# Optimization experiments

Measured on AMD Instinct MI355X. Metric: run time of the kernel, lower is better.

## Reference

```python
import jax, jax.numpy as jnp
import numpy as np

B, T = 32, 64
STOCH, DETER, HIDDEN = 1024, 4096, 1024
ACT_DIM, EMBED = 128, 1536
MIN_STD = 0.1
EPS = 1e-3  # dreamerv3-torch uses LayerNorm(eps=1e-3)


def _ln(x, g, b):
    m = jnp.mean(x, -1, keepdims=True)
    v = jnp.var(x, -1, keepdims=True)
    return (x - m) * jax.lax.rsqrt(v + EPS) * g + b


def setup_inputs() -> dict:
    key = jax.random.key(0)
    ks = jax.random.split(key, 24)

    def w(k, fan_in, fan_out):
        return jax.random.normal(k, (fan_in, fan_out), jnp.float32) / np.sqrt(fan_in)

    inp = {
        "embed": jax.random.normal(ks[0], (B, T, EMBED), jnp.float32),
        "action": jax.random.normal(ks[1], (B, T, ACT_DIM), jnp.float32),
        "is_first": jnp.zeros((B, T), jnp.bool_),
        "init_deter": jax.random.normal(ks[2], (B, DETER), jnp.float32),
        "init_stoch": jax.random.normal(ks[3], (B, STOCH), jnp.float32),
        "noise_prior": jax.random.normal(ks[4], (B, T, STOCH), jnp.float32),
        "noise_post": jax.random.normal(ks[5], (B, T, STOCH), jnp.float32),
        # _img_in_layers: Linear(stoch+act -> hidden, no bias) + LN + SiLU
        "W_in": w(ks[6], STOCH + ACT_DIM, HIDDEN),
        "g_in": 1.0 + 0.1 * jax.random.normal(ks[7], (HIDDEN,), jnp.float32),
        "b_in": 0.1 * jax.random.normal(ks[8], (HIDDEN,), jnp.float32),
        # GRUCell: Linear(hidden+deter -> 3*deter, no bias) + LN
        "W_gru": w(ks[9], HIDDEN + DETER, 3 * DETER),
        "g_gru": 1.0 + 0.1 * jax.random.normal(ks[10], (3 * DETER,), jnp.float32),
        "b_gru": 0.1 * jax.random.normal(ks[11], (3 * DETER,), jnp.float32),
        # _img_out_layers: Linear(deter -> hidden, no bias) + LN + SiLU
        "W_imgout": w(ks[12], DETER, HIDDEN),
        "g_io": 1.0 + 0.1 * jax.random.normal(ks[13], (HIDDEN,), jnp.float32),
        "b_io": 0.1 * jax.random.normal(ks[14], (HIDDEN,), jnp.float32),
        # _obs_out_layers: Linear(deter+embed -> hidden, no bias) + LN + SiLU
        "W_obsout": w(ks[15], DETER + EMBED, HIDDEN),
        "g_oo": 1.0 + 0.1 * jax.random.normal(ks[16], (HIDDEN,), jnp.float32),
        "b_oo": 0.1 * jax.random.normal(ks[17], (HIDDEN,), jnp.float32),
        # suff-stats layers: Linear(hidden -> 2*stoch) with bias
        "W_ims": w(ks[18], HIDDEN, 2 * STOCH),
        "b_ims": 0.01 * jax.random.normal(ks[19], (2 * STOCH,), jnp.float32),
        "W_obs": w(ks[20], HIDDEN, 2 * STOCH),
        "b_obs": 0.01 * jax.random.normal(ks[21], (2 * STOCH,), jnp.float32),
    }
    return inp


def _observe(embed, action, init_deter, init_stoch, noise_prior, noise_post,
             W_in, g_in, b_in, W_gru, g_gru, b_gru, W_imgout, g_io, b_io,
             W_obsout, g_oo, b_oo, W_ims, b_ims, W_obs, b_obs):
    def suff_stats(h, W, b, noise):
        stats = h @ W + b
        mean, std = jnp.split(stats, 2, -1)
        std = jax.nn.softplus(std) + MIN_STD  # std_act='softplus', mean_act='none'
        return mean, std, mean + std * noise

    def step(carry, xs):
        deter, stoch = carry
        e, a, n_p, n_q = xs
        # img_in: concat(prev_stoch, action) -> Linear -> LN -> SiLU
        x = jax.nn.silu(_ln(jnp.concatenate([stoch, a], -1) @ W_in, g_in, b_in))
        # GRUCell with layernorm (update_bias = -1)
        parts = _ln(jnp.concatenate([x, deter], -1) @ W_gru, g_gru, b_gru)
        reset, cand, update = jnp.split(parts, 3, -1)
        reset = jax.nn.sigmoid(reset)
        cand = jnp.tanh(reset * cand)
        update = jax.nn.sigmoid(update - 1.0)
        deter = update * cand + (1.0 - update) * deter
        # prior (imagination) suff stats + sample
        h_p = jax.nn.silu(_ln(deter @ W_imgout, g_io, b_io))
        mean_p, std_p, stoch_p = suff_stats(h_p, W_ims, b_ims, n_p)
        # posterior (observation) suff stats + sample
        h_q = jax.nn.silu(_ln(jnp.concatenate([deter, e], -1) @ W_obsout, g_oo, b_oo))
        mean_q, std_q, stoch_q = suff_stats(h_q, W_obs, b_obs, n_q)
        out = jnp.concatenate([deter, stoch_q, mean_q, std_q, stoch_p, mean_p, std_p], -1)
        return (deter, stoch_q), out

    xs = (jnp.swapaxes(embed, 0, 1), jnp.swapaxes(action, 0, 1),
          jnp.swapaxes(noise_prior, 0, 1), jnp.swapaxes(noise_post, 0, 1))
    _, outs = jax.lax.scan(step, (init_deter, init_stoch), xs)
    return jnp.swapaxes(outs, 0, 1)  # [B, T, deter + 6*stoch]


def reference(embed, action, is_first, init_deter, init_stoch, noise_prior, noise_post,
              W_in, g_in, b_in, W_gru, g_gru, b_gru, W_imgout, g_io, b_io,
              W_obsout, g_oo, b_oo, W_ims, b_ims, W_obs, b_obs):
    # is_first is all-False and state is given, so the init-mixing branch is never taken
    del is_first
    return _observe(embed, action, init_deter, init_stoch, noise_prior, noise_post,
                    W_in, g_in, b_in, W_gru, g_gru, b_gru, W_imgout, g_io, b_io,
                    W_obsout, g_oo, b_oo, W_ims, b_ims, W_obs, b_obs)
```

## Files before the change

kernel.cpp:

```cpp
#include <hip/hip_runtime.h>
#include <hip/hip_bf16.h>

#define T_ 64
#define DETER_ 4096
#define GRUN 12288

typedef __attribute__((ext_vector_type(8))) __bf16 bf16x8;
typedef __attribute__((ext_vector_type(4))) float f32x4;
typedef __attribute__((ext_vector_type(8))) unsigned short u16x8;
typedef __attribute__((ext_vector_type(4))) unsigned short u16x4;

__device__ inline unsigned short f2bf(float f) {
    union { float f; unsigned u; } x; x.f = f;
    unsigned r = x.u + 0x7fffu + ((x.u >> 16) & 1u);
    return (unsigned short)(r >> 16);
}
__device__ inline float sigmoidf_(float v) { return 1.f / (1.f + __expf(-v)); }
__device__ inline float siluf_(float v)    { return v / (1.f + __expf(-v)); }
__device__ inline float softplusf_(float v){ return fmaxf(v, 0.f) + __logf(1.f + __expf(-fabsf(v))); }
__device__ inline float tanhf_(float v)    { return 2.f / (1.f + __expf(-2.f * v)) - 1.f; }

__device__ inline void barrier_() {
    asm volatile("" ::: "memory");
    __builtin_amdgcn_s_barrier();
    asm volatile("" ::: "memory");
}
template <int N> __device__ inline void vmwaitN() {
    asm volatile("s_waitcnt vmcnt(%0)" :: "i"(N) : "memory");
}
__device__ inline void lgkmwait_() {
    asm volatile("s_waitcnt lgkmcnt(0)" ::: "memory");
}


__global__ __launch_bounds__(256) void k_pack(const float* __restrict__ W,
                                              unsigned short* __restrict__ dst,
                                              int K, int N) {
    long fid = (long)blockIdx.x * 256 + threadIdx.x;
    long nfr = (long)K * N / 8;
    if (fid >= nfr) return;
    int lane = (int)(fid & 63);
    long tile = fid >> 6;
    int ktiles = K >> 5;
    int k_t = (int)(tile % ktiles);
    int n_t = (int)(tile / ktiles);
    int c = lane & 15, kb = lane >> 4;
    int k0 = k_t * 32 + kb * 8;
    int n = n_t * 16 + c;
    unsigned short v[8];
#pragma unroll
    for (int i = 0; i < 8; i++) v[i] = f2bf(W[(long)(k0 + i) * N + n]);
    *reinterpret_cast<u16x8*>(dst + fid * 8) = *reinterpret_cast<u16x8*>(v);
}

__global__ __launch_bounds__(256) void k_conv(const float* __restrict__ s,
                                              unsigned short* __restrict__ d, long n) {
    long i = ((long)blockIdx.x * 256 + threadIdx.x) * 4;
    if (i >= n) return;
    f32x4 v = *reinterpret_cast<const f32x4*>(s + i);
    unsigned short o[4];
#pragma unroll
    for (int k = 0; k < 4; k++) o[k] = f2bf(v[k]);
    *reinterpret_cast<u16x4*>(d + i) = *reinterpret_cast<u16x4*>(o);
}

__global__ __launch_bounds__(256) void k_copy(const float* __restrict__ s,
                                              float* __restrict__ d, long n) {
    long i = ((long)blockIdx.x * 256 + threadIdx.x) * 4;
    if (i >= n) return;
    *reinterpret_cast<f32x4*>(d + i) = *reinterpret_cast<const f32x4*>(s + i);
}


template <int CW>
__device__ inline void stage_glds(unsigned short* chunk, const unsigned short* __restrict__ src,
                                  long ld, long k0) {
    constexpr int NI = (32 * CW * 2) / 4096;
    int wv = (int)threadIdx.x >> 6, lane = (int)threadIdx.x & 63;
#pragma unroll
    for (int i = 0; i < NI; ++i) {
        int obase = (wv * NI + i) << 10;
        int o = obase + lane * 16;
        int row = o / (CW * 2);
        int cb = o - row * (CW * 2);
        int gb = cb ^ ((row & 7) << 4);
        const char* ga = (const char*)(src + (long)row * ld + k0) + gb;
        __builtin_amdgcn_global_load_lds(
            (const __attribute__((address_space(1))) void*)ga,
            (__attribute__((address_space(3))) void*)(chunk + (obase >> 1)),
            16, 0, 0);
    }
}

__device__ inline void stage_ln512(unsigned short* chunk, const float* __restrict__ raw,
                                   int ld, int col0,
                                   const float* __restrict__ g, const float* __restrict__ b,
                                   const float* s_mean, const float* s_rstd) {
    int tid = threadIdx.x;
#pragma unroll
    for (int i = 0; i < 8; ++i) {
        int e = tid * 8 + i * 2048;
        int row = e >> 9, col = e & 511;
        float m = s_mean[row], rs = s_rstd[row];
        const float* sp = raw + (long)row * ld + col0 + col;
        unsigned short pk[8];
#pragma unroll
        for (int j = 0; j < 8; ++j) {
            float ln = (sp[j] - m) * rs * g[col0 + col + j] + b[col0 + col + j];
            pk[j] = f2bf(siluf_(ln));
        }
        int dcol = col ^ ((row & 7) << 3);
        *reinterpret_cast<u16x8*>(chunk + row * 512 + dcol) = *reinterpret_cast<u16x8*>(pk);
    }
}

__device__ inline void stage_lnsum(unsigned short* chunk, const float* __restrict__ hpart,
                                   const float* __restrict__ eprep, int t, int col0,
                                   const float* __restrict__ g, const float* __restrict__ b,
                                   const float* s_mean, const float* s_rstd) {
    int tid = threadIdx.x;
#pragma unroll
    for (int i = 0; i < 8; ++i) {
        int e = tid * 8 + i * 2048;
        int row = e >> 9, col = e & 511;
        int k = col0 + col;
        float m = s_mean[row], rs = s_rstd[row];
        const float* h0 = hpart + (long)row * 1024 + k;
        const float* ep = eprep + ((long)row * T_ + t) * 1024 + k;
        unsigned short pk[8];
#pragma unroll
        for (int jj = 0; jj < 8; jj += 4) {
            f32x4 v = *reinterpret_cast<const f32x4*>(h0 + jj);
            v += *reinterpret_cast<const f32x4*>(h0 + 32768 + jj);
            v += *reinterpret_cast<const f32x4*>(h0 + 65536 + jj);
            v += *reinterpret_cast<const f32x4*>(h0 + 98304 + jj);
            v += *reinterpret_cast<const f32x4*>(ep + jj);
#pragma unroll
            for (int j2 = 0; j2 < 4; ++j2) {
                float ln = (v[j2] - m) * rs * g[k + jj + j2] + b[k + jj + j2];
                pk[jj + j2] = f2bf(siluf_(ln));
            }
        }
        int dcol = col ^ ((row & 7) << 3);
        *reinterpret_cast<u16x8*>(chunk + row * 512 + dcol) = *reinterpret_cast<u16x8*>(pk);
    }
}

template <int CW>
__device__ inline void mfma_rh(const unsigned short* chunk, int row, int kb,
                               const unsigned short* __restrict__ bp, f32x4& acc) {
    constexpr int NKT = CW / 32;
    const unsigned short* ap = chunk + row * CW;
    int sw = (row & 7) << 3;
#pragma unroll
    for (int kt = 0; kt < NKT; ++kt) {
        bf16x8 a = *reinterpret_cast<const bf16x8*>(ap + ((kb * 8 + kt * 32) ^ sw));
        bf16x8 b = *reinterpret_cast<const bf16x8*>(bp + (long)kt * 512);
        acc = __builtin_amdgcn_mfma_f32_16x16x32_bf16(a, b, acc, 0, 0, 0);
    }
}

template <int CW>
__device__ inline void mfma2(const unsigned short* chunk, int c, int kb,
                             const unsigned short* __restrict__ bp,
                             f32x4& acc0, f32x4& acc1) {
    constexpr int NKT = CW / 32;
    const unsigned short* ap0 = chunk + c * CW;
    const unsigned short* ap1 = chunk + (16 + c) * CW;
    int sw = (c & 7) << 3;
#pragma unroll
    for (int kt = 0; kt < NKT; ++kt) {
        int off = (kb * 8 + kt * 32) ^ sw;
        bf16x8 b = *reinterpret_cast<const bf16x8*>(bp + (long)kt * 512);
        bf16x8 a0 = *reinterpret_cast<const bf16x8*>(ap0 + off);
        bf16x8 a1 = *reinterpret_cast<const bf16x8*>(ap1 + off);
        acc0 = __builtin_amdgcn_mfma_f32_16x16x32_bf16(a0, b, acc0, 0, 0, 0);
        acc1 = __builtin_amdgcn_mfma_f32_16x16x32_bf16(a1, b, acc1, 0, 0, 0);
    }
}

template <int CW, int NG, int NL>
__global__ __launch_bounds__(256) void k_gemm32(
    const unsigned short* __restrict__ Bp, int Ktiles, int ktg0,
    const unsigned short* __restrict__ srcA, long ldA,
    const float* __restrict__ lnraw, int lnld,
    const float* __restrict__ g_ln, const float* __restrict__ b_ln,
    const float* __restrict__ pstats, int nslab_in,
    const float* __restrict__ addin, long addin_ld,
    float* __restrict__ outp, long out_ld,
    float* __restrict__ partials, long prows)
{
    constexpr int NCH = NG + NL;
    constexpr int NI = (32 * CW * 2) / 4096;
    __shared__ __align__(16) unsigned short sb[2][32 * CW];
    __shared__ float s_out[32][34];
    __shared__ float s_mean[32], s_rstd[32];
    int tid = threadIdx.x;
    if (NL > 0) {
        if (tid < 32) {
            float s = 0.f, q = 0.f;
            for (int j = 0; j < nslab_in; ++j) {
                s += pstats[((long)j * 32 + tid) * 2];
                q += pstats[((long)j * 32 + tid) * 2 + 1];
            }
            float m = s * (1.f / 1024.f);
            s_mean[tid] = m;
            s_rstd[tid] = rsqrtf(q * (1.f / 1024.f) - m * m + 1e-3f);
        }
        __syncthreads();
    }
    int rowbase = blockIdx.y * 32;
    const unsigned short* srcAr = srcA + (long)rowbase * ldA;
    int lane = tid & 63, wv = tid >> 6;
    int nt = wv >> 1, rh = wv & 1;
    int c = lane & 15, kb = lane >> 4;
    int mrow = rh * 16 + c;
    long ntg = (long)blockIdx.x * 2 + nt;
    const unsigned short* bbase = Bp + (long)ntg * Ktiles * 512 + lane * 8;
    f32x4 acc = {0.f, 0.f, 0.f, 0.f};
    stage_glds<CW>(sb[0], srcAr, ldA, 0);
    for (int ch = 0; ch < NCH; ++ch) {
        int nx = ch + 1;
        if (nx < NG) stage_glds<CW>(sb[nx & 1], srcAr, ldA, (long)nx * CW);
        else if (nx < NCH) stage_ln512(sb[nx & 1], lnraw, lnld, (nx - NG) * 512,
                                       g_ln, b_ln, s_mean, s_rstd);
        if (ch < NG) { if (nx < NG) vmwaitN<NI>(); else vmwaitN<0>(); }
        if (nx >= NG && nx < NCH) lgkmwait_();
        barrier_();
        int kt0 = (ch < NG) ? (ktg0 + ch * (CW / 32)) : ((ch - NG) * 16);
        mfma_rh<CW>(sb[ch & 1], mrow, kb, bbase + (long)kt0 * 512, acc);
        barrier_();
    }
    __syncthreads();
#pragma unroll
    for (int j = 0; j < 4; ++j) s_out[rh * 16 + kb * 4 + j][nt * 16 + c] = acc[j];
    __syncthreads();
    int orow = tid >> 3, c4 = (tid & 7) * 4;
    long rg = rowbase + orow;
    float v[4]; float s = 0.f, q = 0.f;
#pragma unroll
    for (int i = 0; i < 4; ++i) {
        float x = s_out[orow][c4 + i];
        if (addin) x += addin[rg * addin_ld + blockIdx.x * 32 + c4 + i];
        v[i] = x; s += x; q += x * x;
    }
#pragma unroll
    for (int i = 0; i < 4; ++i) outp[rg * out_ld + blockIdx.x * 32 + c4 + i] = v[i];
    if (partials) {
#pragma unroll
        for (int m = 1; m < 8; m <<= 1) { s += __shfl_xor(s, m); q += __shfl_xor(q, m); }
        if ((tid & 7) == 0) {
            partials[((long)blockIdx.x * prows + rg) * 2] = s;
            partials[((long)blockIdx.x * prows + rg) * 2 + 1] = q;
        }
    }
}

__global__ __launch_bounds__(256) void k_gru2(
    const unsigned short* __restrict__ Bp,
    const unsigned short* __restrict__ deterb,
    const float* __restrict__ x_raw, const float* __restrict__ px,
    const float* __restrict__ g_in, const float* __restrict__ b_in,
    float* __restrict__ Gp0, float* __restrict__ Gp1)
{
    __shared__ __align__(16) unsigned short sb[2][32 * 512];
    __shared__ float s_out[32][66];
    __shared__ float s_mean[32], s_rstd[32];
    int tid = threadIdx.x, lane = tid & 63, wv = tid >> 6;
    int c = lane & 15, kb = lane >> 4;
    long ntg = (long)blockIdx.x * 4 + wv;
    const unsigned short* bbase = Bp + ntg * 160 * 512 + lane * 8;
    f32x4 acc0 = {0,0,0,0}, acc1 = {0,0,0,0};

    if (blockIdx.y == 0) {
        if (tid < 32) {
            float s = 0.f, q = 0.f;
            for (int j = 0; j < 32; ++j) {
                s += px[((long)j * 32 + tid) * 2];
                q += px[((long)j * 32 + tid) * 2 + 1];
            }
            float m = s * (1.f / 1024.f);
            s_mean[tid] = m;
            s_rstd[tid] = rsqrtf(q * (1.f / 1024.f) - m * m + 1e-3f);
        }
        __syncthreads();
        stage_glds<512>(sb[0], deterb, 4096, 0);
        stage_glds<512>(sb[1], deterb, 4096, 512);
        vmwaitN<8>(); barrier_();
        mfma2<512>(sb[0], c, kb, bbase + 32 * 512, acc0, acc1);
        barrier_();
        stage_glds<512>(sb[0], deterb, 4096, 1024);
        vmwaitN<8>(); barrier_();
        mfma2<512>(sb[1], c, kb, bbase + 48 * 512, acc0, acc1);
        barrier_();
        stage_ln512(sb[1], x_raw, 1024, 0, g_in, b_in, s_mean, s_rstd);
        vmwaitN<0>(); barrier_();
        mfma2<512>(sb[0], c, kb, bbase + 64 * 512, acc0, acc1);
        barrier_();
        stage_ln512(sb[0], x_raw, 1024, 512, g_in, b_in, s_mean, s_rstd);
        lgkmwait_(); barrier_();
        mfma2<512>(sb[1], c, kb, bbase + 0, acc0, acc1);
        barrier_();
        mfma2<512>(sb[0], c, kb, bbase + 16 * 512, acc0, acc1);
    } else {
        stage_glds<512>(sb[0], deterb, 4096, 1536);
        stage_glds<512>(sb[1], deterb, 4096, 2048);
        vmwaitN<8>(); barrier_();
        mfma2<512>(sb[0], c, kb, bbase + 80 * 512, acc0, acc1);
        barrier_();
        stage_glds<512>(sb[0], deterb, 4096, 2560);
        vmwaitN<8>(); barrier_();
        mfma2<512>(sb[1], c, kb, bbase + 96 * 512, acc0, acc1);
        barrier_();
        stage_glds<512>(sb[1], deterb, 4096, 3072);
        vmwaitN<8>(); barrier_();
        mfma2<512>(sb[0], c, kb, bbase + 112 * 512, acc0, acc1);
        barrier_();
        stage_glds<512>(sb[0], deterb, 4096, 3584);
        vmwaitN<8>(); barrier_();
        mfma2<512>(sb[1], c, kb, bbase + 128 * 512, acc0, acc1);
        barrier_();
        vmwaitN<0>(); barrier_();
        mfma2<512>(sb[0], c, kb, bbase + 144 * 512, acc0, acc1);
    }
    __syncthreads();
#pragma unroll
    for (int j = 0; j < 4; ++j) {
        s_out[kb * 4 + j][wv * 16 + c] = acc0[j];
        s_out[16 + kb * 4 + j][wv * 16 + c] = acc1[j];
    }
    __syncthreads();
    float* G = (blockIdx.y == 0) ? Gp0 : Gp1;
    int row = tid >> 3, c8 = (tid & 7) * 8;
#pragma unroll
    for (int i = 0; i < 8; ++i)
        G[(long)row * GRUN + blockIdx.x * 64 + c8 + i] = s_out[row][c8 + i];
}

__global__ __launch_bounds__(1024) void k_deter2(
    const float* __restrict__ Gp0, const float* __restrict__ Gp1,
    const float* __restrict__ g_gru, const float* __restrict__ b_gru,
    float* __restrict__ deterf, unsigned short* __restrict__ deterb,
    unsigned short* __restrict__ deter_allb, float* __restrict__ out, int t)
{
    __shared__ float gsh[GRUN];
    __shared__ float red[32];
    int r = blockIdx.x, tid = threadIdx.x;
    int lane = tid & 63, wv = tid >> 6;
    const float* a0 = Gp0 + (long)r * GRUN;
    const float* a1 = Gp1 + (long)r * GRUN;
    float s = 0.f, q = 0.f;
#pragma unroll
    for (int i = 0; i < 3; ++i) {
        int col = (tid + i * 1024) * 4;
        f32x4 v = *reinterpret_cast<const f32x4*>(a0 + col);
        v += *reinterpret_cast<const f32x4*>(a1 + col);
        *reinterpret_cast<f32x4*>(gsh + col) = v;
#pragma unroll
        for (int j = 0; j < 4; ++j) { s += v[j]; q += v[j] * v[j]; }
    }
#pragma unroll
    for (int m = 1; m < 64; m <<= 1) { s += __shfl_xor(s, m); q += __shfl_xor(q, m); }
    if (lane == 0) { red[wv] = s; red[16 + wv] = q; }
    __syncthreads();
    float fs = 0.f, fq = 0.f;
#pragma unroll
    for (int i = 0; i < 16; ++i) { fs += red[i]; fq += red[16 + i]; }
    float mean = fs * (1.f / 12288.f);
    float rstd = rsqrtf(fq * (1.f / 12288.f) - mean * mean + 1e-3f);
    long orow = (long)r * T_ + t;
#pragma unroll
    for (int it = 0; it < 2; ++it) {
        int j = tid * 2 + it * 2048;
        float2 rr = *reinterpret_cast<const float2*>(gsh + j);
        float2 cc = *reinterpret_cast<const float2*>(gsh + 4096 + j);
        float2 uu = *reinterpret_cast<const float2*>(gsh + 8192 + j);
        float2 dd = *reinterpret_cast<const float2*>(deterf + (long)r * DETER_ + j);
        float dn[2]; unsigned short db[2];
#pragma unroll
        for (int i = 0; i < 2; ++i) {
            float gv = (i == 0) ? rr.x : rr.y;
            float cv = (i == 0) ? cc.x : cc.y;
            float uv = (i == 0) ? uu.x : uu.y;
            float dv = (i == 0) ? dd.x : dd.y;
            float lr = (gv - mean) * rstd * g_gru[j + i] + b_gru[j + i];
            float lc = (cv - mean) * rstd * g_gru[4096 + j + i] + b_gru[4096 + j + i];
            float lu = (uv - mean) * rstd * g_gru[8192 + j + i] + b_gru[8192 + j + i];
            float reset = sigmoidf_(lr);
            float cand = tanhf_(reset * lc);
            float upd = sigmoidf_(lu - 1.f);
            dn[i] = upd * cand + (1.f - upd) * dv;
            db[i] = f2bf(dn[i]);
        }
        float2 nd; nd.x = dn[0]; nd.y = dn[1];
        *reinterpret_cast<float2*>(deterf + (long)r * DETER_ + j) = nd;
        unsigned pk = (unsigned)db[0] | ((unsigned)db[1] << 16);
        *reinterpret_cast<unsigned*>(deterb + (long)r * DETER_ + j) = pk;
        *reinterpret_cast<unsigned*>(deter_allb + orow * DETER_ + j) = pk;
        *reinterpret_cast<float2*>(out + orow * 10240 + j) = nd;
    }
}

__global__ __launch_bounds__(256) void k_h4(
    const unsigned short* __restrict__ Wood,
    const unsigned short* __restrict__ deterb,
    float* __restrict__ hpart)
{
    __shared__ __align__(16) unsigned short sb[2][32 * 512];
    __shared__ float s_out[32][66];
    int tid = threadIdx.x, lane = tid & 63, wv = tid >> 6;
    int c = lane & 15, kb = lane >> 4;
    int n = blockIdx.x, kq = blockIdx.y;
    const unsigned short* bbase = Wood + ((long)(n * 4 + wv) * 128) * 512 + lane * 8;
    f32x4 acc0 = {0,0,0,0}, acc1 = {0,0,0,0};
    stage_glds<512>(sb[0], deterb, 4096, (long)kq * 1024);
    stage_glds<512>(sb[1], deterb, 4096, (long)kq * 1024 + 512);
    vmwaitN<8>(); barrier_();
    mfma2<512>(sb[0], c, kb, bbase + (long)(kq * 32) * 512, acc0, acc1);
    vmwaitN<0>(); barrier_();
    mfma2<512>(sb[1], c, kb, bbase + (long)(kq * 32 + 16) * 512, acc0, acc1);
    __syncthreads();
#pragma unroll
    for (int j = 0; j < 4; ++j) {
        s_out[kb * 4 + j][wv * 16 + c] = acc0[j];
        s_out[16 + kb * 4 + j][wv * 16 + c] = acc1[j];
    }
    __syncthreads();
    int row = tid >> 3, c8 = (tid & 7) * 8;
    float* hp = hpart + (long)kq * 32768 + (long)row * 1024 + n * 64 + c8;
#pragma unroll
    for (int i = 0; i < 8; ++i) hp[i] = s_out[row][c8 + i];
}

__global__ __launch_bounds__(256) void k_statsq2(
    const unsigned short* __restrict__ Bp, const float* __restrict__ hpart,
    const float* __restrict__ E_pre,
    const float* __restrict__ g_oo, const float* __restrict__ b_oo,
    const float* __restrict__ bias,
    const float* __restrict__ noise, float* __restrict__ out,
    unsigned short* __restrict__ stochb, int t)
{
    __shared__ __align__(16) unsigned short sb[2][32 * 512];
    __shared__ float s_out[32][66];
    __shared__ float s_mean[32], s_rstd[32];
    int tid = threadIdx.x, lane = tid & 63, wv = tid >> 6;
    int c = lane & 15, kb = lane >> 4;
    {
        int row = tid >> 3, c0 = (tid & 7) * 128;
        const float* h0 = hpart + (long)row * 1024 + c0;
        const float* ep = E_pre + ((long)row * T_ + t) * 1024 + c0;
        float s = 0.f, q = 0.f;
#pragma unroll 8
        for (int kk = 0; kk < 128; kk += 4) {
            f32x4 v = *reinterpret_cast<const f32x4*>(h0 + kk);
            v += *reinterpret_cast<const f32x4*>(h0 + 32768 + kk);
            v += *reinterpret_cast<const f32x4*>(h0 + 65536 + kk);
            v += *reinterpret_cast<const f32x4*>(h0 + 98304 + kk);
            v += *reinterpret_cast<const f32x4*>(ep + kk);
#pragma unroll
            for (int j2 = 0; j2 < 4; ++j2) { s += v[j2]; q += v[j2] * v[j2]; }
        }
#pragma unroll
        for (int m = 1; m < 8; m <<= 1) { s += __shfl_xor(s, m); q += __shfl_xor(q, m); }
        if ((tid & 7) == 0) {
            float mm = s * (1.f / 1024.f);
            s_mean[row] = mm;
            s_rstd[row] = rsqrtf(q * (1.f / 1024.f) - mm * mm + 1e-3f);
        }
    }
    __syncthreads();
    int part = wv >> 1, nt = wv & 1;
    long ntg = (long)part * 64 + blockIdx.x * 2 + nt;
    const unsigned short* bbase = Bp + ntg * 32 * 512 + lane * 8;
    f32x4 acc0 = {0,0,0,0}, acc1 = {0,0,0,0};
    stage_lnsum(sb[0], hpart, E_pre, t, 0, g_oo, b_oo, s_mean, s_rstd);
    stage_lnsum(sb[1], hpart, E_pre, t, 512, g_oo, b_oo, s_mean, s_rstd);
    lgkmwait_(); barrier_();
    mfma2<512>(sb[0], c, kb, bbase, acc0, acc1);
    mfma2<512>(sb[1], c, kb, bbase + 16 * 512, acc0, acc1);
    __syncthreads();
    float bv = bias[ntg * 16 + c];
#pragma unroll
    for (int j = 0; j < 4; ++j) {
        s_out[kb * 4 + j][part * 32 + nt * 16 + c] = acc0[j] + bv;
        s_out[16 + kb * 4 + j][part * 32 + nt * 16 + c] = acc1[j] + bv;
    }
    __syncthreads();
    int r = tid >> 3, j0 = (tid & 7) * 4;
    long orow = (long)r * T_ + t;
#pragma unroll
    for (int i = 0; i < 4; ++i) {
        int j = j0 + i;
        float mean = s_out[r][j];
        float sd = softplusf_(s_out[r][32 + j]) + 0.1f;
        int cg2 = blockIdx.x * 32 + j;
        float st = mean + sd * noise[orow * 1024 + cg2];
        float* op = out + orow * 10240;
        op[4096 + cg2] = st; op[5120 + cg2] = mean; op[6144 + cg2] = sd;
        stochb[(long)r * 1024 + cg2] = f2bf(st);
    }
}

__global__ __launch_bounds__(256) void k_bstats(
    const unsigned short* __restrict__ Bp, const unsigned short* __restrict__ h_pb,
    const float* __restrict__ bias, const float* __restrict__ noise,
    float* __restrict__ out)
{
    __shared__ __align__(16) unsigned short sb[2][32 * 512];
    __shared__ float s_out[32][66];
    int tid = threadIdx.x;
    int lane = tid & 63, wv = tid >> 6;
    int part = wv >> 1, nt = wv & 1;
    int c = lane & 15, kb = lane >> 4;
    int s_ = blockIdx.x, rowbase = blockIdx.y * 32;
    const unsigned short* A = h_pb + (long)rowbase * 1024;
    long ntg = (long)part * 64 + s_ * 2 + nt;
    const unsigned short* bbase = Bp + ntg * 32 * 512 + lane * 8;
    f32x4 acc0 = {0.f,0.f,0.f,0.f}, acc1 = {0.f,0.f,0.f,0.f};
    stage_glds<512>(sb[0], A, 1024, 0);
    stage_glds<512>(sb[1], A, 1024, 512);
    vmwaitN<8>(); barrier_();
    mfma_rh<512>(sb[0], c, kb, bbase, acc0);
    mfma_rh<512>(sb[0], 16 + c, kb, bbase, acc1);
    vmwaitN<0>(); barrier_();
    mfma_rh<512>(sb[1], c, kb, bbase + 16 * 512, acc0);
    mfma_rh<512>(sb[1], 16 + c, kb, bbase + 16 * 512, acc1);
    __syncthreads();
    float bv = bias[ntg * 16 + c];
#pragma unroll
    for (int j = 0; j < 4; ++j) {
        s_out[kb * 4 + j][part * 32 + nt * 16 + c] = acc0[j] + bv;
        s_out[16 + kb * 4 + j][part * 32 + nt * 16 + c] = acc1[j] + bv;
    }
    __syncthreads();
    int r = tid >> 3, j0 = (tid & 7) * 4;
    long orow = rowbase + r;
#pragma unroll
    for (int i = 0; i < 4; ++i) {
        int j = j0 + i;
        float mean = s_out[r][j];
        float sd = softplusf_(s_out[r][32 + j]) + 0.1f;
        int cg2 = s_ * 32 + j;
        float st = mean + sd * noise[orow * 1024 + cg2];
        float* op = out + orow * 10240;
        op[7168 + cg2] = st; op[8192 + cg2] = mean; op[9216 + cg2] = sd;
    }
}

__global__ __launch_bounds__(256) void k_bfin(const float* __restrict__ hp_raw,
                                              const float* __restrict__ pbh,
                                              const float* __restrict__ g_io,
                                              const float* __restrict__ b_io,
                                              unsigned short* __restrict__ h_pb) {
    int row = blockIdx.x * 8 + ((int)threadIdx.x >> 5);
    int l = threadIdx.x & 31;
    float s = pbh[((long)l * 2048 + row) * 2];
    float q = pbh[((long)l * 2048 + row) * 2 + 1];
#pragma unroll
    for (int m = 16; m; m >>= 1) { s += __shfl_xor(s, m, 32); q += __shfl_xor(q, m, 32); }
    float mn = s * (1.f / 1024.f);
    float rs = rsqrtf(q * (1.f / 1024.f) - mn * mn + 1e-3f);
#pragma unroll
    for (int i = 0; i < 8; ++i) {
        int col = i * 128 + l * 4;
        f32x4 v = *reinterpret_cast<const f32x4*>(hp_raw + (long)row * 1024 + col);
        unsigned short pk[4];
#pragma unroll
        for (int j = 0; j < 4; ++j) {
            float ln = (v[j] - mn) * rs * g_io[col + j] + b_io[col + j];
            pk[j] = f2bf(siluf_(ln));
        }
        *reinterpret_cast<u16x4*>(h_pb + (long)row * 1024 + col) = *reinterpret_cast<u16x4*>(pk);
    }
}


extern "C" void kernel_launch(void* const* d_in, const int* in_sizes, int n_in,
                              void* d_out, int out_size, void* d_ws, size_t ws_size,
                              hipStream_t stream) {
    const float* embed      = (const float*)d_in[0];
    const float* action     = (const float*)d_in[1];
    const float* init_deter = (const float*)d_in[3];
    const float* init_stoch = (const float*)d_in[4];
    const float* noise_pr   = (const float*)d_in[5];
    const float* noise_po   = (const float*)d_in[6];
    const float* W_in       = (const float*)d_in[7];
    const float* g_in       = (const float*)d_in[8];
    const float* b_in       = (const float*)d_in[9];
    const float* W_gru      = (const float*)d_in[10];
    const float* g_gru      = (const float*)d_in[11];
    const float* b_gru      = (const float*)d_in[12];
    const float* W_io       = (const float*)d_in[13];
    const float* g_io       = (const float*)d_in[14];
    const float* b_io       = (const float*)d_in[15];
    const float* W_oo       = (const float*)d_in[16];
    const float* g_oo       = (const float*)d_in[17];
    const float* b_oo       = (const float*)d_in[18];
    const float* W_ims      = (const float*)d_in[19];
    const float* b_ims      = (const float*)d_in[20];
    const float* W_obs      = (const float*)d_in[21];
    const float* b_obs      = (const float*)d_in[22];
    float* out = (float*)d_out;

    char* ws = (char*)d_ws;
    size_t off = 0;
    auto alloc = [&](size_t bytes) {
        size_t r = off;
        off = (off + bytes + 255) & ~(size_t)255;
        return r;
    };
    unsigned short* pWgru  = (unsigned short*)(ws + alloc((size_t)5120 * 12288 * 2));
    unsigned short* pWin_s = (unsigned short*)(ws + alloc((size_t)1024 * 1024 * 2));
    unsigned short* pWin_a = (unsigned short*)(ws + alloc((size_t)128 * 1024 * 2));
    unsigned short* pWio   = (unsigned short*)(ws + alloc((size_t)4096 * 1024 * 2));
    unsigned short* pWood  = (unsigned short*)(ws + alloc((size_t)4096 * 1024 * 2));
    unsigned short* pWooe  = (unsigned short*)(ws + alloc((size_t)1536 * 1024 * 2));
    unsigned short* pWims  = (unsigned short*)(ws + alloc((size_t)1024 * 2048 * 2));
    unsigned short* pWobs  = (unsigned short*)(ws + alloc((size_t)1024 * 2048 * 2));
    unsigned short* act_bf = (unsigned short*)(ws + alloc((size_t)2048 * 128 * 2));
    unsigned short* emb_bf = (unsigned short*)(ws + alloc((size_t)2048 * 1536 * 2));
    float* A_pre  = (float*)(ws + alloc((size_t)2048 * 1024 * 4));
    float* E_pre  = (float*)(ws + alloc((size_t)2048 * 1024 * 4));
    float* x_raw  = (float*)(ws + alloc((size_t)32 * 1024 * 4));
    float* Gp0    = (float*)(ws + alloc((size_t)32 * GRUN * 4));
    float* Gp1    = (float*)(ws + alloc((size_t)32 * GRUN * 4));
    float* deterf = (float*)(ws + alloc((size_t)32 * DETER_ * 4));
    unsigned short* deterb     = (unsigned short*)(ws + alloc((size_t)32 * DETER_ * 2));
    unsigned short* deter_allb = (unsigned short*)(ws + alloc((size_t)2048 * DETER_ * 2));
    unsigned short* stochb = (unsigned short*)(ws + alloc((size_t)32 * 1024 * 2));
    float* hp_raw = (float*)(ws + alloc((size_t)2048 * 1024 * 4));
    unsigned short* h_pb = (unsigned short*)(ws + alloc((size_t)2048 * 1024 * 2));
    float* px  = (float*)(ws + alloc((size_t)32 * 32 * 2 * 4));
    float* pbh = (float*)(ws + alloc((size_t)32 * 2048 * 2 * 4));
    float* hpart = (float*)(ws + alloc((size_t)4 * 32 * 1024 * 4));
    (void)ws_size; (void)out_size; (void)n_in; (void)in_sizes;

    auto packgrid = [](long K, long N) { return (unsigned)((K * N / 8 + 255) / 256); };

    k_pack<<<packgrid(5120, 12288), 256, 0, stream>>>(W_gru, pWgru, 5120, 12288);
    k_pack<<<packgrid(1024, 1024), 256, 0, stream>>>(W_in, pWin_s, 1024, 1024);
    k_pack<<<packgrid(128, 1024), 256, 0, stream>>>(W_in + (size_t)1024 * 1024, pWin_a, 128, 1024);
    k_pack<<<packgrid(4096, 1024), 256, 0, stream>>>(W_io, pWio, 4096, 1024);
    k_pack<<<packgrid(4096, 1024), 256, 0, stream>>>(W_oo, pWood, 4096, 1024);
    k_pack<<<packgrid(1536, 1024), 256, 0, stream>>>(W_oo + (size_t)4096 * 1024, pWooe, 1536, 1024);
    k_pack<<<packgrid(1024, 2048), 256, 0, stream>>>(W_ims, pWims, 1024, 2048);
    k_pack<<<packgrid(1024, 2048), 256, 0, stream>>>(W_obs, pWobs, 1024, 2048);
    k_conv<<<(2048 * 128 / 4 + 255) / 256, 256, 0, stream>>>(action, act_bf, 2048L * 128);
    k_conv<<<(2048 * 1536 / 4 + 255) / 256, 256, 0, stream>>>(embed, emb_bf, 2048L * 1536);
    k_conv<<<(32 * 1024 / 4 + 255) / 256, 256, 0, stream>>>(init_stoch, stochb, 32L * 1024);
    k_conv<<<(32 * 4096 / 4 + 255) / 256, 256, 0, stream>>>(init_deter, deterb, 32L * 4096);
    k_copy<<<(32 * 4096 / 4 + 255) / 256, 256, 0, stream>>>(init_deter, deterf, 32L * 4096);
    k_gemm32<128, 1, 0><<<dim3(32, 64), 256, 0, stream>>>(
        pWin_a, 4, 0, act_bf, 128, nullptr, 0, nullptr, nullptr, nullptr, 0,
        nullptr, 0, A_pre, 1024, nullptr, 0);
    k_gemm32<512, 3, 0><<<dim3(32, 64), 256, 0, stream>>>(
        pWooe, 48, 0, emb_bf, 1536, nullptr, 0, nullptr, nullptr, nullptr, 0,
        nullptr, 0, E_pre, 1024, nullptr, 0);

    for (int t = 0; t < T_; ++t) {
        k_gemm32<512, 2, 0><<<dim3(32, 1), 256, 0, stream>>>(
            pWin_s, 32, 0, stochb, 1024, nullptr, 0, nullptr, nullptr, nullptr, 0,
            A_pre + (size_t)t * 1024, (long)T_ * 1024, x_raw, 1024, px, 32);
        k_gru2<<<dim3(192, 2), 256, 0, stream>>>(pWgru, deterb, x_raw, px, g_in, b_in,
                                                 Gp0, Gp1);
        k_deter2<<<32, 1024, 0, stream>>>(Gp0, Gp1, g_gru, b_gru, deterf, deterb,
                                          deter_allb, out, t);
        k_h4<<<dim3(16, 4), 256, 0, stream>>>(pWood, deterb, hpart);
        k_statsq2<<<32, 256, 0, stream>>>(pWobs, hpart, E_pre, g_oo, b_oo, b_obs,
                                          noise_po, out, stochb, t);
    }

    k_gemm32<512, 8, 0><<<dim3(32, 64), 256, 0, stream>>>(
        pWio, 128, 0, deter_allb, 4096, nullptr, 0, nullptr, nullptr, nullptr, 0,
        nullptr, 0, hp_raw, 1024, pbh, 2048);
    k_bfin<<<256, 256, 0, stream>>>(hp_raw, pbh, g_io, b_io, h_pb);
    k_bstats<<<dim3(32, 64), 256, 0, stream>>>(pWims, h_pb, b_ims, noise_pr, out);
}
```

Before: 7.000 ms.

## Replace per-timestep kernel launches with persistent cooperative megakernel using flag sync

Swaps the 64×5 per-step kernel launches of the recurrent loop for one persistent cooperative kernel of 256 blocks. Blocks take specialised roles (GRU GEMM, deter update, posterior stats plus next-step input GEMM) and hand off through global atomic flags instead of kernel boundaries. The deter-dependent part of the next GRU GEMM and the stoch input GEMM can now overlap with other stages. The goal is to remove launch and kernel-drain overhead on a latency-bound scan. The cost is spin-wait polling, a dependence on every block being co-resident, and a fallback path if the cooperative launch fails.

```diff
diff --git a/kernel.cpp b/kernel.cpp
--- a/kernel.cpp
+++ b/kernel.cpp
@@ -30,6 +30,19 @@
 }
 __device__ inline void lgkmwait_() {
     asm volatile("s_waitcnt lgkmcnt(0)" ::: "memory");
+}
+
+__device__ inline void waitflag(int* f, int target) {
+    if (threadIdx.x == 0) {
+        while (__hip_atomic_load(f, __ATOMIC_ACQUIRE, __HIP_MEMORY_SCOPE_AGENT) < target)
+            __builtin_amdgcn_s_sleep(2);
+    }
+    __syncthreads();
+}
+__device__ inline void postflag(int* f) {
+    __syncthreads();
+    if (threadIdx.x == 0)
+        __hip_atomic_fetch_add(f, 1, __ATOMIC_RELEASE, __HIP_MEMORY_SCOPE_AGENT);
 }
 
 
@@ -71,6 +84,11 @@
     *reinterpret_cast<f32x4*>(d + i) = *reinterpret_cast<const f32x4*>(s + i);
 }
 
+__global__ void k_zeroflags(int* f, int n) {
+    int i = blockIdx.x * 256 + threadIdx.x;
+    if (i < n) f[i] = 0;
+}
+
 
 template <int CW>
 __device__ inline void stage_glds(unsigned short* chunk, const unsigned short* __restrict__ src,
@@ -178,6 +196,292 @@
         acc1 = __builtin_amdgcn_mfma_f32_16x16x32_bf16(a1, b, acc1, 0, 0, 0);
     }
 }
+
+struct MArgs {
+    const unsigned short *pWin_s, *pWgru, *pWood, *pWobs;
+    const float *A_pre, *E_pre;
+    const float *g_in, *b_in, *g_gru, *b_gru, *g_oo, *b_oo, *b_obs;
+    const float *noise_po;
+    unsigned short *stochb, *deterb, *deter_allb;
+    float *deterf, *x_raw, *px, *G_raw, *hpart, *out;
+    int *fX, *fG, *fD, *fH, *fS;
+};
+
+__global__ __launch_bounds__(256, 1) void k_mega(MArgs a) {
+    __shared__ __align__(16) char smem[74240];
+    unsigned short (*sb)[32 * 512] = reinterpret_cast<unsigned short(*)[32 * 512]>(smem);
+    float (*s_out)[66] = reinterpret_cast<float(*)[66]>(smem + 65536);
+    float* s_mean = reinterpret_cast<float*>(smem + 65536 + 8448);
+    float* s_rstd = s_mean + 32;
+    float* gsh = reinterpret_cast<float*>(smem);
+    float* red = reinterpret_cast<float*>(smem + 49152);
+
+    int bid = blockIdx.x, tid = threadIdx.x;
+    int lane = tid & 63, wv = tid >> 6;
+    int c = lane & 15, kb = lane >> 4;
+
+    if (bid < 192) {
+        long ntg = (long)bid * 4 + wv;
+        const unsigned short* bbase = a.pWgru + ntg * 160 * 512 + lane * 8;
+        const unsigned short* hbase = nullptr;
+        int hn = bid & 15, hkq = bid >> 4;
+        if (bid < 64)
+            hbase = a.pWood + ((long)(hn * 4 + wv) * 128) * 512 + lane * 8;
+        for (int t = 0; t < T_; ++t) {
+            if (t > 0) waitflag(&a.fD[t - 1], 32);
+            f32x4 acc0 = {0, 0, 0, 0}, acc1 = {0, 0, 0, 0};
+            stage_glds<512>(sb[0], a.deterb, 4096, 0);
+            stage_glds<512>(sb[1], a.deterb, 4096, 512);
+#pragma unroll
+            for (int ch = 0; ch < 8; ++ch) {
+                if (ch < 7) vmwaitN<8>(); else vmwaitN<0>();
+                barrier_();
+                mfma2<512>(sb[ch & 1], c, kb, bbase + (long)(32 + ch * 16) * 512, acc0, acc1);
+                barrier_();
+                if (ch < 6) stage_glds<512>(sb[ch & 1], a.deterb, 4096, (long)(ch + 2) * 512);
+            }
+            waitflag(&a.fX[t], 16);
+            if (tid < 32) {
+                float s = 0.f, q = 0.f;
+                for (int j = 0; j < 16; ++j) {
+                    s += a.px[((long)j * 32 + tid) * 2];
+                    q += a.px[((long)j * 32 + tid) * 2 + 1];
+                }
+                float m = s * (1.f / 1024.f);
+                s_mean[tid] = m;
+                s_rstd[tid] = rsqrtf(q * (1.f / 1024.f) - m * m + 1e-3f);
+            }
+            __syncthreads();
+            stage_ln512(sb[0], a.x_raw, 1024, 0, a.g_in, a.b_in, s_mean, s_rstd);
+            stage_ln512(sb[1], a.x_raw, 1024, 512, a.g_in, a.b_in, s_mean, s_rstd);
+            lgkmwait_(); barrier_();
+            mfma2<512>(sb[0], c, kb, bbase, acc0, acc1);
+            mfma2<512>(sb[1], c, kb, bbase + (long)16 * 512, acc0, acc1);
+            __syncthreads();
+#pragma unroll
+            for (int j = 0; j < 4; ++j) {
+                s_out[kb * 4 + j][wv * 16 + c] = acc0[j];
+                s_out[16 + kb * 4 + j][wv * 16 + c] = acc1[j];
+            }
+            __syncthreads();
+            {
+                int row = tid >> 3, c8 = (tid & 7) * 8;
+#pragma unroll
+                for (int i = 0; i < 8; ++i)
+                    a.G_raw[(long)row * GRUN + bid * 64 + c8 + i] = s_out[row][c8 + i];
+            }
+            postflag(&a.fG[t]);
+
+            if (bid < 64) {
+                waitflag(&a.fD[t], 32);
+                f32x4 hacc0 = {0, 0, 0, 0}, hacc1 = {0, 0, 0, 0};
+                stage_glds<512>(sb[0], a.deterb, 4096, (long)hkq * 1024);
+                stage_glds<512>(sb[1], a.deterb, 4096, (long)hkq * 1024 + 512);
+                vmwaitN<8>(); barrier_();
+                mfma2<512>(sb[0], c, kb, hbase + (long)(hkq * 32) * 512, hacc0, hacc1);
+                vmwaitN<0>(); barrier_();
+                mfma2<512>(sb[1], c, kb, hbase + (long)(hkq * 32 + 16) * 512, hacc0, hacc1);
+                __syncthreads();
+#pragma unroll
+                for (int j = 0; j < 4; ++j) {
+                    s_out[kb * 4 + j][wv * 16 + c] = hacc0[j];
+                    s_out[16 + kb * 4 + j][wv * 16 + c] = hacc1[j];
+                }
+                __syncthreads();
+                int row = tid >> 3, c8 = (tid & 7) * 8;
+                float* hp = a.hpart + (long)hkq * 32768 + (long)row * 1024 + hn * 64 + c8;
+#pragma unroll
+                for (int i = 0; i < 8; ++i) hp[i] = s_out[row][c8 + i];
+                postflag(&a.fH[t]);
+            }
+        }
+    } else if (bid < 224) {
+        int r = bid - 192;
+        for (int t = 0; t < T_; ++t) {
+            waitflag(&a.fG[t], 192);
+            const float* g0 = a.G_raw + (long)r * GRUN;
+            float s = 0.f, q = 0.f;
+#pragma unroll
+            for (int i = 0; i < 12; ++i) {
+                int col = tid * 4 + i * 1024;
+                f32x4 v = *reinterpret_cast<const f32x4*>(g0 + col);
+                *reinterpret_cast<f32x4*>(gsh + col) = v;
+#pragma unroll
+                for (int j = 0; j < 4; ++j) { s += v[j]; q += v[j] * v[j]; }
+            }
+#pragma unroll
+            for (int m = 1; m < 64; m <<= 1) { s += __shfl_xor(s, m); q += __shfl_xor(q, m); }
+            if (lane == 0) { red[wv] = s; red[4 + wv] = q; }
+            __syncthreads();
+            float fs = red[0] + red[1] + red[2] + red[3];
+            float fq = red[4] + red[5] + red[6] + red[7];
+            float mean = fs * (1.f / 12288.f);
+            float rstd = rsqrtf(fq * (1.f / 12288.f) - mean * mean + 1e-3f);
+            long orow = (long)r * T_ + t;
+#pragma unroll
+            for (int it = 0; it < 4; ++it) {
+                int j = tid * 4 + it * 1024;
+                f32x4 rr = *reinterpret_cast<const f32x4*>(gsh + j);
+                f32x4 cc = *reinterpret_cast<const f32x4*>(gsh + 4096 + j);
+                f32x4 uu = *reinterpret_cast<const f32x4*>(gsh + 8192 + j);
+                f32x4 dd = *reinterpret_cast<const f32x4*>(a.deterf + (long)r * DETER_ + j);
+                f32x4 nd; unsigned short db[4];
+#pragma unroll
+                for (int i = 0; i < 4; ++i) {
+                    float lr = (rr[i] - mean) * rstd * a.g_gru[j + i] + a.b_gru[j + i];
+                    float lc = (cc[i] - mean) * rstd * a.g_gru[4096 + j + i] + a.b_gru[4096 + j + i];
+                    float lu = (uu[i] - mean) * rstd * a.g_gru[8192 + j + i] + a.b_gru[8192 + j + i];
+                    float reset = sigmoidf_(lr);
+                    float cand = tanhf_(reset * lc);
+                    float upd = sigmoidf_(lu - 1.f);
+                    nd[i] = upd * cand + (1.f - upd) * dd[i];
+                    db[i] = f2bf(nd[i]);
+                }
+                *reinterpret_cast<f32x4*>(a.deterf + (long)r * DETER_ + j) = nd;
+                *reinterpret_cast<u16x4*>(a.deterb + (long)r * DETER_ + j) = *reinterpret_cast<u16x4*>(db);
+                *reinterpret_cast<u16x4*>(a.deter_allb + orow * DETER_ + j) = *reinterpret_cast<u16x4*>(db);
+                *reinterpret_cast<f32x4*>(a.out + orow * 10240 + j) = nd;
+            }
+            postflag(&a.fD[t]);
+        }
+    } else {
+        int s_ = bid - 224;
+        int part = wv >> 1, nt = wv & 1;
+        long ntg = (long)part * 64 + s_ * 2 + nt;
+        const unsigned short* bbase = a.pWobs + ntg * 32 * 512 + lane * 8;
+        const unsigned short* xbase = nullptr;
+        if (s_ < 16)
+            xbase = a.pWin_s + ((long)s_ * 4 + wv) * 32 * 512 + lane * 8;
+
+        if (s_ < 16) {
+            f32x4 xa0 = {0, 0, 0, 0}, xa1 = {0, 0, 0, 0};
+            stage_glds<512>(sb[0], a.stochb, 1024, 0);
+            stage_glds<512>(sb[1], a.stochb, 1024, 512);
+            vmwaitN<8>(); barrier_();
+            mfma2<512>(sb[0], c, kb, xbase, xa0, xa1);
+            vmwaitN<0>(); barrier_();
+            mfma2<512>(sb[1], c, kb, xbase + (long)16 * 512, xa0, xa1);
+            __syncthreads();
+#pragma unroll
+            for (int j = 0; j < 4; ++j) {
+                s_out[kb * 4 + j][wv * 16 + c] = xa0[j];
+                s_out[16 + kb * 4 + j][wv * 16 + c] = xa1[j];
+            }
+            __syncthreads();
+            int row = tid >> 3, c8 = (tid & 7) * 8;
+            const float* ap = a.A_pre + ((long)row * T_ + 0) * 1024 + s_ * 64 + c8;
+            float s = 0.f, q = 0.f, v[8];
+#pragma unroll
+            for (int i = 0; i < 8; ++i) {
+                float x = s_out[row][c8 + i] + ap[i];
+                v[i] = x; s += x; q += x * x;
+            }
+#pragma unroll
+            for (int i = 0; i < 8; ++i) a.x_raw[(long)row * 1024 + s_ * 64 + c8 + i] = v[i];
+#pragma unroll
+            for (int m = 1; m < 8; m <<= 1) { s += __shfl_xor(s, m); q += __shfl_xor(q, m); }
+            if ((tid & 7) == 0) {
+                a.px[((long)s_ * 32 + row) * 2] = s;
+                a.px[((long)s_ * 32 + row) * 2 + 1] = q;
+            }
+            postflag(&a.fX[0]);
+        }
+
+        for (int t = 0; t < T_; ++t) {
+            waitflag(&a.fH[t], 64);
+            {
+                int row = tid >> 3, c0 = (tid & 7) * 128;
+                const float* h0 = a.hpart + (long)row * 1024 + c0;
+                const float* ep = a.E_pre + ((long)row * T_ + t) * 1024 + c0;
+                float s = 0.f, q = 0.f;
+#pragma unroll 8
+                for (int kk = 0; kk < 128; kk += 4) {
+                    f32x4 v = *reinterpret_cast<const f32x4*>(h0 + kk);
+                    v += *reinterpret_cast<const f32x4*>(h0 + 32768 + kk);
+                    v += *reinterpret_cast<const f32x4*>(h0 + 65536 + kk);
+                    v += *reinterpret_cast<const f32x4*>(h0 + 98304 + kk);
+                    v += *reinterpret_cast<const f32x4*>(ep + kk);
+#pragma unroll
+                    for (int j2 = 0; j2 < 4; ++j2) { s += v[j2]; q += v[j2] * v[j2]; }
+                }
+#pragma unroll
+                for (int m = 1; m < 8; m <<= 1) { s += __shfl_xor(s, m); q += __shfl_xor(q, m); }
+                if ((tid & 7) == 0) {
+                    float mm = s * (1.f / 1024.f);
+                    s_mean[row] = mm;
+                    s_rstd[row] = rsqrtf(q * (1.f / 1024.f) - mm * mm + 1e-3f);
+                }
+            }
+            __syncthreads();
+            f32x4 acc0 = {0, 0, 0, 0}, acc1 = {0, 0, 0, 0};
+            stage_lnsum(sb[0], a.hpart, a.E_pre, t, 0, a.g_oo, a.b_oo, s_mean, s_rstd);
+            stage_lnsum(sb[1], a.hpart, a.E_pre, t, 512, a.g_oo, a.b_oo, s_mean, s_rstd);
+            lgkmwait_(); barrier_();
+            mfma2<512>(sb[0], c, kb, bbase, acc0, acc1);
+            mfma2<512>(sb[1], c, kb, bbase + (long)16 * 512, acc0, acc1);
+            __syncthreads();
+            float bv = a.b_obs[ntg * 16 + c];
+#pragma unroll
+            for (int j = 0; j < 4; ++j) {
+                s_out[kb * 4 + j][part * 32 + nt * 16 + c] = acc0[j] + bv;
+                s_out[16 + kb * 4 + j][part * 32 + nt * 16 + c] = acc1[j] + bv;
+            }
+            __syncthreads();
+            {
+                int r = tid >> 3, j0 = (tid & 7) * 4;
+                long orow = (long)r * T_ + t;
+#pragma unroll
+                for (int i = 0; i < 4; ++i) {
+                    int j = j0 + i;
+                    float mean = s_out[r][j];
+                    float sd = softplusf_(s_out[r][32 + j]) + 0.1f;
+                    int cg2 = s_ * 32 + j;
+                    float st = mean + sd * a.noise_po[orow * 1024 + cg2];
+                    float* op = a.out + orow * 10240;
+                    op[4096 + cg2] = st; op[5120 + cg2] = mean; op[6144 + cg2] = sd;
+                    a.stochb[(long)r * 1024 + cg2] = f2bf(st);
+                }
+            }
+            postflag(&a.fS[t]);
+
+            if (s_ < 16 && t + 1 < T_) {
+                waitflag(&a.fS[t], 32);
+                f32x4 xa0 = {0, 0, 0, 0}, xa1 = {0, 0, 0, 0};
+                stage_glds<512>(sb[0], a.stochb, 1024, 0);
+                stage_glds<512>(sb[1], a.stochb, 1024, 512);
+                vmwaitN<8>(); barrier_();
+                mfma2<512>(sb[0], c, kb, xbase, xa0, xa1);
+                vmwaitN<0>(); barrier_();
+                mfma2<512>(sb[1], c, kb, xbase + (long)16 * 512, xa0, xa1);
+                __syncthreads();
+#pragma unroll
+                for (int j = 0; j < 4; ++j) {
+                    s_out[kb * 4 + j][wv * 16 + c] = xa0[j];
+                    s_out[16 + kb * 4 + j][wv * 16 + c] = xa1[j];
+                }
+                __syncthreads();
+                int row = tid >> 3, c8 = (tid & 7) * 8;
+                const float* ap = a.A_pre + ((long)row * T_ + (t + 1)) * 1024 + s_ * 64 + c8;
+                float s = 0.f, q = 0.f, v[8];
+#pragma unroll
+                for (int i = 0; i < 8; ++i) {
+                    float x = s_out[row][c8 + i] + ap[i];
+                    v[i] = x; s += x; q += x * x;
+                }
+#pragma unroll
+                for (int i = 0; i < 8; ++i) a.x_raw[(long)row * 1024 + s_ * 64 + c8 + i] = v[i];
+#pragma unroll
+                for (int m = 1; m < 8; m <<= 1) { s += __shfl_xor(s, m); q += __shfl_xor(q, m); }
+                if ((tid & 7) == 0) {
+                    a.px[((long)s_ * 32 + row) * 2] = s;
+                    a.px[((long)s_ * 32 + row) * 2 + 1] = q;
+                }
+                postflag(&a.fX[t + 1]);
+            }
+        }
+    }
+}
+
 
 template <int CW, int NG, int NL>
 __global__ __launch_bounds__(256) void k_gemm32(
@@ -633,6 +937,7 @@
     float* px  = (float*)(ws + alloc((size_t)32 * 32 * 2 * 4));
     float* pbh = (float*)(ws + alloc((size_t)32 * 2048 * 2 * 4));
     float* hpart = (float*)(ws + alloc((size_t)4 * 32 * 1024 * 4));
+    int* flags = (int*)(ws + alloc((size_t)5 * 64 * 4));
     (void)ws_size; (void)out_size; (void)n_in; (void)in_sizes;
 
     auto packgrid = [](long K, long N) { return (unsigned)((K * N / 8 + 255) / 256); };
@@ -656,18 +961,36 @@
     k_gemm32<512, 3, 0><<<dim3(32, 64), 256, 0, stream>>>(
         pWooe, 48, 0, emb_bf, 1536, nullptr, 0, nullptr, nullptr, nullptr, 0,
         nullptr, 0, E_pre, 1024, nullptr, 0);
-
-    for (int t = 0; t < T_; ++t) {
-        k_gemm32<512, 2, 0><<<dim3(32, 1), 256, 0, stream>>>(
-            pWin_s, 32, 0, stochb, 1024, nullptr, 0, nullptr, nullptr, nullptr, 0,
-            A_pre + (size_t)t * 1024, (long)T_ * 1024, x_raw, 1024, px, 32);
-        k_gru2<<<dim3(192, 2), 256, 0, stream>>>(pWgru, deterb, x_raw, px, g_in, b_in,
-                                                 Gp0, Gp1);
-        k_deter2<<<32, 1024, 0, stream>>>(Gp0, Gp1, g_gru, b_gru, deterf, deterb,
-                                          deter_allb, out, t);
-        k_h4<<<dim3(16, 4), 256, 0, stream>>>(pWood, deterb, hpart);
-        k_statsq2<<<32, 256, 0, stream>>>(pWobs, hpart, E_pre, g_oo, b_oo, b_obs,
-                                          noise_po, out, stochb, t);
+    k_zeroflags<<<2, 256, 0, stream>>>(flags, 5 * 64);
+
+    MArgs ma;
+    ma.pWin_s = pWin_s; ma.pWgru = pWgru; ma.pWood = pWood; ma.pWobs = pWobs;
+    ma.A_pre = A_pre; ma.E_pre = E_pre;
+    ma.g_in = g_in; ma.b_in = b_in; ma.g_gru = g_gru; ma.b_gru = b_gru;
+    ma.g_oo = g_oo; ma.b_oo = b_oo; ma.b_obs = b_obs;
+    ma.noise_po = noise_po;
+    ma.stochb = stochb; ma.deterb = deterb; ma.deter_allb = deter_allb;
+    ma.deterf = deterf; ma.x_raw = x_raw; ma.px = px;
+    ma.G_raw = Gp0; ma.hpart = hpart; ma.out = out;
+    ma.fX = flags; ma.fG = flags + 64; ma.fD = flags + 128;
+    ma.fH = flags + 192; ma.fS = flags + 256;
+    void* kargs[] = { &ma };
+    hipError_t rc = hipLaunchCooperativeKernel((const void*)k_mega, dim3(256), dim3(256),
+                                               kargs, 0, stream);
+    if (rc != hipSuccess) {
+        (void)hipGetLastError();
+        for (int t = 0; t < T_; ++t) {
+            k_gemm32<512, 2, 0><<<dim3(32, 1), 256, 0, stream>>>(
+                pWin_s, 32, 0, stochb, 1024, nullptr, 0, nullptr, nullptr, nullptr, 0,
+                A_pre + (size_t)t * 1024, (long)T_ * 1024, x_raw, 1024, px, 32);
+            k_gru2<<<dim3(192, 2), 256, 0, stream>>>(pWgru, deterb, x_raw, px, g_in, b_in,
+                                                     Gp0, Gp1);
+            k_deter2<<<32, 1024, 0, stream>>>(Gp0, Gp1, g_gru, b_gru, deterf, deterb,
+                                              deter_allb, out, t);
+            k_h4<<<dim3(16, 4), 256, 0, stream>>>(pWood, deterb, hpart);
+            k_statsq2<<<32, 256, 0, stream>>>(pWobs, hpart, E_pre, g_oo, b_oo, b_obs,
+                                              noise_po, out, stochb, t);
+        }
     }
 
     k_gemm32<512, 8, 0><<<dim3(32, 64), 256, 0, stream>>>(
```

Result: slower. 23.84 ms (+240.6%).
